# Kernel tuning notes

Measured on AMD Instinct MI355X. Metric: run time of the kernel, lower is better.

## Reference

```python
import jax, jax.numpy as jnp
import numpy as np

B, S, D, V = 32, 1024, 768, 32000


def setup_inputs() -> dict:
    key = jax.random.key(0)
    ks = jax.random.split(key, 12)
    scale = 0.02
    return {
        "tokens": jax.random.randint(ks[0], (B, S), 0, V, dtype=jnp.int32),
        "mask": jax.random.randint(ks[1], (B, S), 0, 2, dtype=jnp.int32),
        "emb": jax.random.normal(ks[2], (V, D), dtype=jnp.float32) * scale,
        "wq": jax.random.normal(ks[3], (D, D), dtype=jnp.float32) * scale,
        "wk": jax.random.normal(ks[4], (D, D), dtype=jnp.float32) * scale,
        "wv": jax.random.normal(ks[5], (D, D), dtype=jnp.float32) * scale,
        "ln_g": jnp.ones((D,), dtype=jnp.float32),
        "ln_b": jnp.zeros((D,), dtype=jnp.float32),
        "w1": jax.random.normal(ks[6], (D, D), dtype=jnp.float32) * scale,
        "b1": jnp.zeros((D,), dtype=jnp.float32),
        "wh": jax.random.normal(ks[7], (D, 2), dtype=jnp.float32) * scale,
        "bh": jnp.zeros((2,), dtype=jnp.float32),
    }


def reference(tokens, mask, emb, wq, wk, wv, ln_g, ln_b, w1, b1, wh, bh):
    # embedding lookup: [B,S,D]
    x = emb[tokens]
    q = x @ wq
    k = x @ wk
    v = x @ wv
    # unscaled attention scores: [B,S,S]
    s = jnp.einsum("bsd,btd->bst", q, k)
    # additive padding mask (mask==1 -> -1e9), broadcast over query dim
    s = s + (-1e9) * mask.astype(s.dtype)[:, None, :]
    a = jax.nn.softmax(s, axis=-1)
    o = jnp.einsum("bst,btd->bsd", a, v)
    # classify on first token
    cls = o[:, 0, :]  # [B,D]
    mu = jnp.mean(cls, axis=-1, keepdims=True)
    var = jnp.var(cls, axis=-1, keepdims=True)
    h = (cls - mu) * jax.lax.rsqrt(var + 1e-5) * ln_g + ln_b
    h = jax.nn.gelu(h @ w1 + b1, approximate=False)
    logits = h @ wh + bh  # [B,2]
    return (logits, a)
```

## Files before the change

### kernel.cpp

```cpp
#include <hip/hip_runtime.h>
#include <hip/hip_bf16.h>

#define NB 32
#define SS 1024
#define DD 768

typedef __attribute__((ext_vector_type(8))) short bf16x8;
typedef __attribute__((ext_vector_type(4))) float f32x4;

__device__ inline ushort f2bf(float f) {
    union { float f; unsigned u; } x;
    x.f = f;
    unsigned r = (x.u + 0x7fffu + ((x.u >> 16) & 1u)) >> 16;
    return (ushort)r;
}

#define GLOBAL_PTR(x) ((const __attribute__((address_space(1))) void*)(x))
#define LDS_PTR(x)    ((__attribute__((address_space(3))) void*)(x))

__global__ void k_cvt(const float* __restrict__ wq, const float* __restrict__ wk,
                      ushort* __restrict__ wqb, ushort* __restrict__ wkb) {
    const int i = (blockIdx.x * 256 + threadIdx.x) * 4;
    const float* src = blockIdx.y ? wk : wq;
    ushort* dst = blockIdx.y ? wkb : wqb;
    const float4 v = *(const float4*)(src + i);
    ushort4 o;
    o.x = f2bf(v.x); o.y = f2bf(v.y); o.z = f2bf(v.z); o.w = f2bf(v.w);
    *(ushort4*)(dst + i) = o;
}

__global__ void k_gather(const int* __restrict__ tokens, const float* __restrict__ emb,
                         ushort* __restrict__ xb) {
    int i = (blockIdx.x * 256 + threadIdx.x) * 4;
    int row = i / DD;
    int col = i - row * DD;
    int tok = tokens[row];
    const float4 v = *(const float4*)(emb + (size_t)tok * DD + col);
    ushort4 o;
    o.x = f2bf(v.x); o.y = f2bf(v.y); o.z = f2bf(v.z); o.w = f2bf(v.w);
    *(ushort4*)(xb + (size_t)row * DD + col) = o;
}

__global__ __launch_bounds__(256, 2) void k_gemm_s(const ushort* __restrict__ A,
                                                   const ushort* __restrict__ Bt,
                                                   ushort* __restrict__ Cb) {
    constexpr int BK = 64;
    __shared__ ushort As[2][128 * BK];
    __shared__ ushort Bs[2][128 * BK];
    const int tid = threadIdx.x;
    const int wave = tid >> 6, lane = tid & 63;
    const int bx = blockIdx.x, by = blockIdx.y;
    const size_t abase = (size_t)bx * 128 * DD;
    const size_t bbase = (size_t)by * 128 * DD;
    const int r = tid >> 3;
    const int cc = (tid & 7) * 8;

    auto stage = [&](int buf, int k0) {
#pragma unroll
        for (int i = 0; i < 4; i++) {
            __builtin_amdgcn_global_load_lds(GLOBAL_PTR(A + abase + (size_t)(r + i * 32) * DD + k0 + cc),
                                             LDS_PTR(&As[buf][(r + i * 32) * BK + cc]), 16, 0, 0);
            __builtin_amdgcn_global_load_lds(GLOBAL_PTR(Bt + bbase + (size_t)(r + i * 32) * DD + k0 + cc),
                                             LDS_PTR(&Bs[buf][(r + i * 32) * BK + cc]), 16, 0, 0);
        }
    };

    f32x4 acc[4][4] = {};
    const int wm = (wave >> 1) * 64, wn = (wave & 1) * 64;
    const int lr = lane & 15, lc = (lane >> 4) * 8;

    stage(0, 0);
    __syncthreads();
    int cur = 0;
#pragma unroll 1
    for (int k0 = 0; k0 < DD; k0 += BK) {
        if (k0 + BK < DD) stage(cur ^ 1, k0 + BK);
        const ushort* as = As[cur];
        const ushort* bs = Bs[cur];
#pragma unroll
        for (int kk = 0; kk < 2; kk++) {
            bf16x8 af[4], bfv[4];
#pragma unroll
            for (int m = 0; m < 4; m++)
                af[m] = *(const bf16x8*)(as + (wm + m * 16 + lr) * BK + kk * 32 + lc);
#pragma unroll
            for (int n = 0; n < 4; n++)
                bfv[n] = *(const bf16x8*)(bs + (wn + n * 16 + lr) * BK + kk * 32 + lc);
#pragma unroll
            for (int m = 0; m < 4; m++)
#pragma unroll
                for (int n = 0; n < 4; n++)
                    acc[m][n] = __builtin_amdgcn_mfma_f32_16x16x32_bf16(af[m], bfv[n], acc[m][n], 0, 0, 0);
        }
        __syncthreads();
        cur ^= 1;
    }
    const int rowbase = bx * 128 + wm + (lane >> 4) * 4;
    const int colbase = by * 128 + wn + (lane & 15);
#pragma unroll
    for (int m = 0; m < 4; m++)
#pragma unroll
        for (int n = 0; n < 4; n++)
#pragma unroll
            for (int j = 0; j < 4; j++)
                Cb[(size_t)(rowbase + m * 16 + j) * DD + colbase + n * 16] = f2bf(acc[m][n][j]);
}

__global__ __launch_bounds__(512) void k_attn(const ushort* __restrict__ Y,
                                              const ushort* __restrict__ X,
                                              const int* __restrict__ mask,
                                              float* __restrict__ Aout) {
    __shared__ ushort Bsh[2][SS * 32];
    __shared__ ushort Ash[2][64 * 32];
    __shared__ int    Msk[SS];
    __shared__ float  RedM[8][64];
    __shared__ float  RedS[8][64];

    const int tid = threadIdx.x;
    const int wid = tid >> 6, lane = tid & 63;
    const int la = lane & 15, lg = lane >> 4;

    const int wgid = blockIdx.x;
    const int g = wgid >> 7, w = wgid & 127;
    const int b = g * 8 + (w & 7);
    const int bx = w >> 3;
    const ushort* Ag = Y + (size_t)b * SS * DD + (size_t)bx * 64 * DD;
    const ushort* Bg = X + (size_t)b * SS * DD;
    float* Ao = Aout + (size_t)b * SS * SS + (size_t)bx * 64 * SS;

    Msk[tid] = mask[b * SS + tid];
    Msk[tid + 512] = mask[b * SS + tid + 512];

    auto stageB = [&](ushort* dst, const ushort* gsrc) {
#pragma unroll
        for (int l = 0; l < 8; l++) {
            const int L = (l * 512 + tid) * 16;
            const int r = L >> 6;
            const int scol = ((L & 63) ^ ((r & 3) << 4)) >> 1;
            __builtin_amdgcn_global_load_lds(GLOBAL_PTR(gsrc + (size_t)r * DD + scol),
                                             LDS_PTR(dst + (L >> 1)), 16, 0, 0);
        }
    };
    auto stageA = [&](ushort* dst, const ushort* gsrc) {
        if (tid < 256) {
            const int L = tid * 16;
            const int r = L >> 6;
            const int scol = ((L & 63) ^ ((r & 3) << 4)) >> 1;
            __builtin_amdgcn_global_load_lds(GLOBAL_PTR(gsrc + (size_t)r * DD + scol),
                                             LDS_PTR(dst + (L >> 1)), 16, 0, 0);
        }
    };

    const int koff = ((lg ^ (la & 3)) << 3);

    f32x4 acc[4][8] = {};

    stageA(&Ash[0][0], Ag);
    stageB(&Bsh[0][0], Bg);
    __syncthreads();

#pragma unroll 1
    for (int t = 0; t < 24; t++) {
        if (t < 23) {
            const int k1 = (t + 1) * 32;
            stageA(&Ash[(t + 1) & 1][0], Ag + k1);
            stageB(&Bsh[(t + 1) & 1][0], Bg + k1);
        }
        const ushort* ash = &Ash[t & 1][0];
        const ushort* bsh = &Bsh[t & 1][0];
        bf16x8 af[4];
#pragma unroll
        for (int m = 0; m < 4; m++)
            af[m] = *(const bf16x8*)(ash + (m * 16 + la) * 32 + koff);
#pragma unroll
        for (int n = 0; n < 8; n++) {
            const bf16x8 bf = *(const bf16x8*)(bsh + (wid * 128 + n * 16 + la) * 32 + koff);
            __builtin_amdgcn_s_setprio(1);
#pragma unroll
            for (int m = 0; m < 4; m++)
                acc[m][n] = __builtin_amdgcn_mfma_f32_16x16x32_bf16(af[m], bf, acc[m][n], 0, 0, 0);
            __builtin_amdgcn_s_setprio(0);
        }
        __syncthreads();
    }

    float bias[8];
#pragma unroll
    for (int n = 0; n < 8; n++)
        bias[n] = Msk[wid * 128 + n * 16 + la] ? -1e9f : 0.0f;

    float mxl[4][4];
#pragma unroll
    for (int m = 0; m < 4; m++)
#pragma unroll
        for (int j = 0; j < 4; j++) {
            float v = -3.4e38f;
#pragma unroll
            for (int n = 0; n < 8; n++) v = fmaxf(v, acc[m][n][j] + bias[n]);
#pragma unroll
            for (int off = 1; off < 16; off <<= 1) v = fmaxf(v, __shfl_xor(v, off));
            mxl[m][j] = v;
        }
    if (la == 0) {
#pragma unroll
        for (int m = 0; m < 4; m++)
#pragma unroll
            for (int j = 0; j < 4; j++)
                RedM[wid][m * 16 + lg * 4 + j] = mxl[m][j];
    }
    __syncthreads();
#pragma unroll
    for (int m = 0; m < 4; m++)
#pragma unroll
        for (int j = 0; j < 4; j++) {
            const int r = m * 16 + lg * 4 + j;
            float v = RedM[0][r];
#pragma unroll
            for (int ww = 1; ww < 8; ww++) v = fmaxf(v, RedM[ww][r]);
            mxl[m][j] = v;
        }

    float sml[4][4];
#pragma unroll
    for (int m = 0; m < 4; m++)
#pragma unroll
        for (int j = 0; j < 4; j++) {
            float s = 0.f;
#pragma unroll
            for (int n = 0; n < 8; n++) {
                const float e = __expf(acc[m][n][j] + bias[n] - mxl[m][j]);
                acc[m][n][j] = e;
                s += e;
            }
#pragma unroll
            for (int off = 1; off < 16; off <<= 1) s += __shfl_xor(s, off);
            sml[m][j] = s;
        }
    if (la == 0) {
#pragma unroll
        for (int m = 0; m < 4; m++)
#pragma unroll
            for (int j = 0; j < 4; j++)
                RedS[wid][m * 16 + lg * 4 + j] = sml[m][j];
    }
    __syncthreads();
#pragma unroll
    for (int m = 0; m < 4; m++)
#pragma unroll
        for (int j = 0; j < 4; j++) {
            const int r = m * 16 + lg * 4 + j;
            float s = RedS[0][r];
#pragma unroll
            for (int ww = 1; ww < 8; ww++) s += RedS[ww][r];
            const float inv = 1.0f / s;
#pragma unroll
            for (int n = 0; n < 8; n++)
                Ao[(size_t)r * SS + wid * 128 + n * 16 + la] = acc[m][n][j] * inv;
        }
}

__global__ __launch_bounds__(256) void k_xbar(const float* __restrict__ a, const int* __restrict__ tokens,
                                              const float* __restrict__ emb, float* __restrict__ part) {
    const int b = blockIdx.x >> 3, c = blockIdx.x & 7;
    __shared__ float a0s[128];
    __shared__ int toks[128];
    const int tid = threadIdx.x;
    if (tid < 128) {
        a0s[tid] = a[(size_t)b * SS * SS + c * 128 + tid];
        toks[tid] = tokens[b * SS + c * 128 + tid];
    }
    __syncthreads();
    float acc0 = 0.f, acc1 = 0.f, acc2 = 0.f;
#pragma unroll 4
    for (int t = 0; t < 128; t++) {
        const float at = a0s[t];
        const float* er = emb + (size_t)toks[t] * DD;
        acc0 = fmaf(at, er[tid], acc0);
        acc1 = fmaf(at, er[tid + 256], acc1);
        acc2 = fmaf(at, er[tid + 512], acc2);
    }
    float* p = part + ((size_t)c * NB + b) * DD;
    p[tid] = acc0; p[tid + 256] = acc1; p[tid + 512] = acc2;
}

__global__ __launch_bounds__(128) void k_cls(const float* __restrict__ part, const float* __restrict__ wv,
                                             float* __restrict__ cls) {
    const int b = blockIdx.y, tid = threadIdx.x;
    const int c = blockIdx.x * 128 + tid;
    __shared__ float xb[DD];
#pragma unroll
    for (int j = 0; j < 6; j++) {
        const int k = tid + j * 128;
        float s = 0.f;
#pragma unroll
        for (int p = 0; p < 8; p++) s += part[((size_t)p * NB + b) * DD + k];
        xb[k] = s;
    }
    __syncthreads();
    float acc = 0.f;
#pragma unroll 8
    for (int k = 0; k < DD; k++) acc = fmaf(xb[k], wv[(size_t)k * DD + c], acc);
    cls[(size_t)b * DD + c] = acc;
}

__device__ inline float block_sum256(float v, float* red, int tid) {
#pragma unroll
    for (int off = 32; off; off >>= 1) v += __shfl_xor(v, off);
    __syncthreads();
    if ((tid & 63) == 0) red[tid >> 6] = v;
    __syncthreads();
    return red[0] + red[1] + red[2] + red[3];
}

__global__ __launch_bounds__(256) void k_ln(const float* __restrict__ cls, const float* __restrict__ ln_g,
                                            const float* __restrict__ ln_b, float* __restrict__ hs) {
    const int b = blockIdx.x, tid = threadIdx.x;
    __shared__ float red[4];
    float v[3];
#pragma unroll
    for (int j = 0; j < 3; j++) v[j] = cls[(size_t)b * DD + tid + j * 256];
    const float mu = block_sum256(v[0] + v[1] + v[2], red, tid) * (1.0f / DD);
    float dv = 0.f;
#pragma unroll
    for (int j = 0; j < 3; j++) { const float d = v[j] - mu; dv += d * d; }
    __syncthreads();
    const float var = block_sum256(dv, red, tid) * (1.0f / DD);
    const float sc = 1.0f / sqrtf(var + 1e-5f);
#pragma unroll
    for (int j = 0; j < 3; j++) {
        const int d = tid + j * 256;
        hs[(size_t)b * DD + d] = (v[j] - mu) * sc * ln_g[d] + ln_b[d];
    }
}

__global__ __launch_bounds__(128) void k_mlp(const float* __restrict__ hs, const float* __restrict__ w1,
                                             const float* __restrict__ b1, const float* __restrict__ wh,
                                             float* __restrict__ part_l) {
    const int b = blockIdx.y, tid = threadIdx.x;
    const int j = blockIdx.x * 128 + tid;
    __shared__ float h[DD];
#pragma unroll
    for (int q = 0; q < 6; q++) h[tid + q * 128] = hs[(size_t)b * DD + tid + q * 128];
    __syncthreads();
    float p = b1[j];
#pragma unroll 8
    for (int d = 0; d < DD; d++) p = fmaf(h[d], w1[(size_t)d * DD + j], p);
    const float g = 0.5f * p * (1.0f + erff(p * 0.70710678118654752f));
    float l0 = g * wh[j * 2 + 0];
    float l1 = g * wh[j * 2 + 1];
#pragma unroll
    for (int off = 32; off; off >>= 1) { l0 += __shfl_xor(l0, off); l1 += __shfl_xor(l1, off); }
    __shared__ float r0[2], r1[2];
    if ((tid & 63) == 0) { r0[tid >> 6] = l0; r1[tid >> 6] = l1; }
    __syncthreads();
    if (tid == 0) {
        part_l[((size_t)b * 6 + blockIdx.x) * 2 + 0] = r0[0] + r0[1];
        part_l[((size_t)b * 6 + blockIdx.x) * 2 + 1] = r1[0] + r1[1];
    }
}

__global__ __launch_bounds__(64) void k_final(const float* __restrict__ part_l, const float* __restrict__ bh,
                                              float* __restrict__ out) {
    const int b = threadIdx.x;
    if (b < NB) {
        float l0 = bh[0], l1 = bh[1];
#pragma unroll
        for (int c = 0; c < 6; c++) {
            l0 += part_l[((size_t)b * 6 + c) * 2 + 0];
            l1 += part_l[((size_t)b * 6 + c) * 2 + 1];
        }
        out[b * 2 + 0] = l0;
        out[b * 2 + 1] = l1;
    }
}

extern "C" void kernel_launch(void* const* d_in, const int* in_sizes, int n_in,
                              void* d_out, int out_size, void* d_ws, size_t ws_size,
                              hipStream_t stream) {
    const int*   tokens = (const int*)d_in[0];
    const int*   mask   = (const int*)d_in[1];
    const float* emb    = (const float*)d_in[2];
    const float* wq     = (const float*)d_in[3];
    const float* wk     = (const float*)d_in[4];
    const float* wv     = (const float*)d_in[5];
    const float* ln_g   = (const float*)d_in[6];
    const float* ln_b   = (const float*)d_in[7];
    const float* w1     = (const float*)d_in[8];
    const float* b1     = (const float*)d_in[9];
    const float* wh     = (const float*)d_in[10];
    const float* bh     = (const float*)d_in[11];
    float* out = (float*)d_out;

    char* ws = (char*)d_ws;
    const size_t XB = (size_t)NB * SS * DD * 2;
    const size_t WB = (size_t)DD * DD * 2;
    ushort* xb  = (ushort*)ws;
    ushort* yb  = (ushort*)(ws + XB);
    ushort* wqb = (ushort*)(ws + 2 * XB);
    ushort* wkb = (ushort*)(ws + 2 * XB + WB);
    ushort* Wt  = (ushort*)(ws + 2 * XB + 2 * WB);
    char*   p4  = ws + 2 * XB + 3 * WB;
    float*  part   = (float*)p4;
    float*  cls    = (float*)(p4 + 786432);
    float*  hsb    = (float*)(p4 + 786432 + 98304);
    float*  part_l = (float*)(p4 + 786432 + 2 * 98304);

    float* a_region = out + 64;

    k_cvt<<<dim3(576, 2), 256, 0, stream>>>(wq, wk, wqb, wkb);
    k_gather<<<24576, 256, 0, stream>>>(tokens, emb, xb);
    k_gemm_s<<<dim3(6, 6), 256, 0, stream>>>(wkb, wqb, Wt);
    k_gemm_s<<<dim3(256, 6), 256, 0, stream>>>(xb, Wt, yb);
    k_attn<<<512, 512, 0, stream>>>(yb, xb, mask, a_region);
    k_xbar<<<256, 256, 0, stream>>>(a_region, tokens, emb, part);
    k_cls<<<dim3(6, NB), 128, 0, stream>>>(part, wv, cls);
    k_ln<<<NB, 256, 0, stream>>>(cls, ln_g, ln_b, hsb);
    k_mlp<<<dim3(6, NB), 128, 0, stream>>>(hsb, w1, b1, wh, part_l);
    k_final<<<1, 64, 0, stream>>>(part_l, bh, out);
}
```

Baseline: 348.8 us.

## Give each wave private LDS buffers and load A fragments directly from global

The QK^T main loop in the attention kernel now has each wave stage only its own 128-row slice of K into a per-wave double-buffered LDS region. Each wave loads its Q fragments straight from global into registers instead of staging them through shared LDS. This replaces the per-iteration workgroup __syncthreads with per-wave vmcnt waits, so waves no longer stall on each other. The trade-off is redundant global reads of the Q tile across the eight waves and more register pressure from two sets of A fragments.

```diff
diff --git a/kernel.cpp b/kernel.cpp
--- a/kernel.cpp
+++ b/kernel.cpp
@@ -110,8 +110,7 @@
                                               const ushort* __restrict__ X,
                                               const int* __restrict__ mask,
                                               float* __restrict__ Aout) {
-    __shared__ ushort Bsh[2][SS * 32];
-    __shared__ ushort Ash[2][64 * 32];
+    __shared__ ushort Bsh[8][2][128 * 32];
     __shared__ int    Msk[SS];
     __shared__ float  RedM[8][64];
     __shared__ float  RedS[8][64];
@@ -125,64 +124,64 @@
     const int b = g * 8 + (w & 7);
     const int bx = w >> 3;
     const ushort* Ag = Y + (size_t)b * SS * DD + (size_t)bx * 64 * DD;
-    const ushort* Bg = X + (size_t)b * SS * DD;
+    const ushort* Bg = X + (size_t)b * SS * DD + (size_t)wid * 128 * DD;
     float* Ao = Aout + (size_t)b * SS * SS + (size_t)bx * 64 * SS;
 
     Msk[tid] = mask[b * SS + tid];
     Msk[tid + 512] = mask[b * SS + tid + 512];
 
-    auto stageB = [&](ushort* dst, const ushort* gsrc) {
-#pragma unroll
-        for (int l = 0; l < 8; l++) {
-            const int L = (l * 512 + tid) * 16;
-            const int r = L >> 6;
-            const int scol = ((L & 63) ^ ((r & 3) << 4)) >> 1;
-            __builtin_amdgcn_global_load_lds(GLOBAL_PTR(gsrc + (size_t)r * DD + scol),
-                                             LDS_PTR(dst + (L >> 1)), 16, 0, 0);
-        }
+    const int sr = lane >> 2;
+    const int scc = ((lane & 3) ^ (sr & 3)) << 3;
+    const int koff = (lg ^ (la & 3)) << 3;
+
+    ushort* wb0 = &Bsh[wid][0][0];
+    ushort* wb1 = &Bsh[wid][1][0];
+
+    auto stageB = [&](ushort* dst, int k0) {
+#pragma unroll
+        for (int i = 0; i < 8; i++)
+            __builtin_amdgcn_global_load_lds(GLOBAL_PTR(Bg + (size_t)(i * 16 + sr) * DD + k0 + scc),
+                                             LDS_PTR(dst + i * 512), 16, 0, 0);
     };
-    auto stageA = [&](ushort* dst, const ushort* gsrc) {
-        if (tid < 256) {
-            const int L = tid * 16;
-            const int r = L >> 6;
-            const int scol = ((L & 63) ^ ((r & 3) << 4)) >> 1;
-            __builtin_amdgcn_global_load_lds(GLOBAL_PTR(gsrc + (size_t)r * DD + scol),
-                                             LDS_PTR(dst + (L >> 1)), 16, 0, 0);
-        }
+    auto loadA = [&](bf16x8* af, int k0) {
+#pragma unroll
+        for (int m = 0; m < 4; m++)
+            af[m] = *(const bf16x8*)(Ag + (size_t)(m * 16 + la) * DD + k0 + lg * 8);
     };
 
-    const int koff = ((lg ^ (la & 3)) << 3);
-
     f32x4 acc[4][8] = {};
-
-    stageA(&Ash[0][0], Ag);
-    stageB(&Bsh[0][0], Bg);
-    __syncthreads();
-
-#pragma unroll 1
-    for (int t = 0; t < 24; t++) {
-        if (t < 23) {
-            const int k1 = (t + 1) * 32;
-            stageA(&Ash[(t + 1) & 1][0], Ag + k1);
-            stageB(&Bsh[(t + 1) & 1][0], Bg + k1);
-        }
-        const ushort* ash = &Ash[t & 1][0];
-        const ushort* bsh = &Bsh[t & 1][0];
-        bf16x8 af[4];
-#pragma unroll
-        for (int m = 0; m < 4; m++)
-            af[m] = *(const bf16x8*)(ash + (m * 16 + la) * 32 + koff);
+    bf16x8 afA[4], afB[4];
+
+    auto comp = [&](const ushort* bsh, const bf16x8* af) {
 #pragma unroll
         for (int n = 0; n < 8; n++) {
-            const bf16x8 bf = *(const bf16x8*)(bsh + (wid * 128 + n * 16 + la) * 32 + koff);
+            const bf16x8 bf = *(const bf16x8*)(bsh + (n * 16 + la) * 32 + koff);
             __builtin_amdgcn_s_setprio(1);
 #pragma unroll
             for (int m = 0; m < 4; m++)
                 acc[m][n] = __builtin_amdgcn_mfma_f32_16x16x32_bf16(af[m], bf, acc[m][n], 0, 0, 0);
             __builtin_amdgcn_s_setprio(0);
         }
-        __syncthreads();
-    }
+    };
+
+    stageB(wb0, 0);
+    loadA(afA, 0);
+    asm volatile("s_waitcnt vmcnt(0)" ::: "memory");
+    __builtin_amdgcn_sched_barrier(0);
+
+#pragma unroll 1
+    for (int tt = 0; tt < 12; tt++) {
+        const int t0 = tt * 2;
+        if (t0 + 1 < 24) { stageB(wb1, (t0 + 1) * 32); loadA(afB, (t0 + 1) * 32); }
+        comp(wb0, afA);
+        asm volatile("s_waitcnt vmcnt(0)" ::: "memory");
+        __builtin_amdgcn_sched_barrier(0);
+        if (t0 + 2 < 24) { stageB(wb0, (t0 + 2) * 32); loadA(afA, (t0 + 2) * 32); }
+        comp(wb1, afB);
+        asm volatile("s_waitcnt vmcnt(0)" ::: "memory");
+        __builtin_amdgcn_sched_barrier(0);
+    }
+    __syncthreads();
 
     float bias[8];
 #pragma unroll
```

New measurement: 344.0 us. Within noise of the previous version (-1.4%).

## Enlarge attention workgroup to 128 query rows with 16 waves sharing K tile

Applied to the files above, without the earlier changes.

The attention score kernel now runs 1024-thread workgroups that each cover 128 query rows instead of 64. Sixteen waves are arranged 2x8 over rows and key columns, so every staged 1024x32 K slice in LDS serves twice as many query rows. This halves the global reloads of the K operand and halves the grid to 256 blocks. The cost is one block per CU with fewer blocks than CUs, less latency hiding across blocks, and larger barriers.

```diff
diff --git a/kernel.cpp b/kernel.cpp
--- a/kernel.cpp
+++ b/kernel.cpp
@@ -106,75 +106,73 @@
                 Cb[(size_t)(rowbase + m * 16 + j) * DD + colbase + n * 16] = f2bf(acc[m][n][j]);
 }
 
-__global__ __launch_bounds__(512) void k_attn(const ushort* __restrict__ Y,
-                                              const ushort* __restrict__ X,
-                                              const int* __restrict__ mask,
-                                              float* __restrict__ Aout) {
+__global__ __launch_bounds__(1024) void k_attn(const ushort* __restrict__ Y,
+                                               const ushort* __restrict__ X,
+                                               const int* __restrict__ mask,
+                                               float* __restrict__ Aout) {
     __shared__ ushort Bsh[2][SS * 32];
-    __shared__ ushort Ash[2][64 * 32];
+    __shared__ ushort Ash[2][128 * 32];
     __shared__ int    Msk[SS];
-    __shared__ float  RedM[8][64];
-    __shared__ float  RedS[8][64];
+    __shared__ float  RedM[8][128];
+    __shared__ float  RedS[8][128];
 
     const int tid = threadIdx.x;
     const int wid = tid >> 6, lane = tid & 63;
     const int la = lane & 15, lg = lane >> 4;
+    const int wm = wid & 1, wn = wid >> 1;
 
     const int wgid = blockIdx.x;
-    const int g = wgid >> 7, w = wgid & 127;
-    const int b = g * 8 + (w & 7);
-    const int bx = w >> 3;
-    const ushort* Ag = Y + (size_t)b * SS * DD + (size_t)bx * 64 * DD;
+    const int x = wgid & 7, k = wgid >> 3;
+    const int b = x + 8 * (k >> 3);
+    const int bx = k & 7;
+    const ushort* Ag = Y + (size_t)b * SS * DD + (size_t)bx * 128 * DD;
     const ushort* Bg = X + (size_t)b * SS * DD;
-    float* Ao = Aout + (size_t)b * SS * SS + (size_t)bx * 64 * SS;
+    float* Ao = Aout + (size_t)b * SS * SS + (size_t)bx * 128 * SS;
 
     Msk[tid] = mask[b * SS + tid];
-    Msk[tid + 512] = mask[b * SS + tid + 512];
-
-    auto stageB = [&](ushort* dst, const ushort* gsrc) {
-#pragma unroll
-        for (int l = 0; l < 8; l++) {
-            const int L = (l * 512 + tid) * 16;
-            const int r = L >> 6;
-            const int scol = ((L & 63) ^ ((r & 3) << 4)) >> 1;
-            __builtin_amdgcn_global_load_lds(GLOBAL_PTR(gsrc + (size_t)r * DD + scol),
-                                             LDS_PTR(dst + (L >> 1)), 16, 0, 0);
+
+    auto stageB = [&](ushort* dst, int k0) {
+#pragma unroll
+        for (int i = 0; i < 4; i++) {
+            const int idx = i * 1024 + tid;
+            const int r = idx >> 2;
+            const int scol = ((idx & 3) ^ (r & 3)) << 3;
+            __builtin_amdgcn_global_load_lds(GLOBAL_PTR(Bg + (size_t)r * DD + k0 + scol),
+                                             LDS_PTR(dst + idx * 8), 16, 0, 0);
         }
     };
-    auto stageA = [&](ushort* dst, const ushort* gsrc) {
-        if (tid < 256) {
-            const int L = tid * 16;
-            const int r = L >> 6;
-            const int scol = ((L & 63) ^ ((r & 3) << 4)) >> 1;
-            __builtin_amdgcn_global_load_lds(GLOBAL_PTR(gsrc + (size_t)r * DD + scol),
-                                             LDS_PTR(dst + (L >> 1)), 16, 0, 0);
+    auto stageA = [&](ushort* dst, int k0) {
+        if (tid < 512) {
+            const int r = tid >> 2;
+            const int scol = ((tid & 3) ^ (r & 3)) << 3;
+            __builtin_amdgcn_global_load_lds(GLOBAL_PTR(Ag + (size_t)r * DD + k0 + scol),
+                                             LDS_PTR(dst + tid * 8), 16, 0, 0);
         }
     };
 
-    const int koff = ((lg ^ (la & 3)) << 3);
+    const int koff = (lg ^ (la & 3)) << 3;
 
     f32x4 acc[4][8] = {};
 
-    stageA(&Ash[0][0], Ag);
-    stageB(&Bsh[0][0], Bg);
+    stageB(&Bsh[0][0], 0);
+    stageA(&Ash[0][0], 0);
     __syncthreads();
 
 #pragma unroll 1
     for (int t = 0; t < 24; t++) {
         if (t < 23) {
-            const int k1 = (t + 1) * 32;
-            stageA(&Ash[(t + 1) & 1][0], Ag + k1);
-            stageB(&Bsh[(t + 1) & 1][0], Bg + k1);
+            stageB(&Bsh[(t + 1) & 1][0], (t + 1) * 32);
+            stageA(&Ash[(t + 1) & 1][0], (t + 1) * 32);
         }
         const ushort* ash = &Ash[t & 1][0];
         const ushort* bsh = &Bsh[t & 1][0];
         bf16x8 af[4];
 #pragma unroll
         for (int m = 0; m < 4; m++)
-            af[m] = *(const bf16x8*)(ash + (m * 16 + la) * 32 + koff);
+            af[m] = *(const bf16x8*)(ash + (wm * 64 + m * 16 + la) * 32 + koff);
 #pragma unroll
         for (int n = 0; n < 8; n++) {
-            const bf16x8 bf = *(const bf16x8*)(bsh + (wid * 128 + n * 16 + la) * 32 + koff);
+            const bf16x8 bf = *(const bf16x8*)(bsh + (wn * 128 + n * 16 + la) * 32 + koff);
             __builtin_amdgcn_s_setprio(1);
 #pragma unroll
             for (int m = 0; m < 4; m++)
@@ -187,7 +185,7 @@
     float bias[8];
 #pragma unroll
     for (int n = 0; n < 8; n++)
-        bias[n] = Msk[wid * 128 + n * 16 + la] ? -1e9f : 0.0f;
+        bias[n] = Msk[wn * 128 + n * 16 + la] ? -1e9f : 0.0f;
 
     float mxl[4][4];
 #pragma unroll
@@ -206,14 +204,14 @@
         for (int m = 0; m < 4; m++)
 #pragma unroll
             for (int j = 0; j < 4; j++)
-                RedM[wid][m * 16 + lg * 4 + j] = mxl[m][j];
+                RedM[wn][wm * 64 + m * 16 + lg * 4 + j] = mxl[m][j];
     }
     __syncthreads();
 #pragma unroll
     for (int m = 0; m < 4; m++)
 #pragma unroll
         for (int j = 0; j < 4; j++) {
-            const int r = m * 16 + lg * 4 + j;
+            const int r = wm * 64 + m * 16 + lg * 4 + j;
             float v = RedM[0][r];
 #pragma unroll
             for (int ww = 1; ww < 8; ww++) v = fmaxf(v, RedM[ww][r]);
@@ -241,21 +239,21 @@
         for (int m = 0; m < 4; m++)
 #pragma unroll
             for (int j = 0; j < 4; j++)
-                RedS[wid][m * 16 + lg * 4 + j] = sml[m][j];
+                RedS[wn][wm * 64 + m * 16 + lg * 4 + j] = sml[m][j];
     }
     __syncthreads();
 #pragma unroll
     for (int m = 0; m < 4; m++)
 #pragma unroll
         for (int j = 0; j < 4; j++) {
-            const int r = m * 16 + lg * 4 + j;
+            const int r = wm * 64 + m * 16 + lg * 4 + j;
             float s = RedS[0][r];
 #pragma unroll
             for (int ww = 1; ww < 8; ww++) s += RedS[ww][r];
             const float inv = 1.0f / s;
 #pragma unroll
             for (int n = 0; n < 8; n++)
-                Ao[(size_t)r * SS + wid * 128 + n * 16 + la] = acc[m][n][j] * inv;
+                Ao[(size_t)r * SS + wn * 128 + n * 16 + la] = acc[m][n][j] * inv;
         }
 }
 
@@ -411,7 +409,7 @@
     k_gather<<<24576, 256, 0, stream>>>(tokens, emb, xb);
     k_gemm_s<<<dim3(6, 6), 256, 0, stream>>>(wkb, wqb, Wt);
     k_gemm_s<<<dim3(256, 6), 256, 0, stream>>>(xb, Wt, yb);
-    k_attn<<<512, 512, 0, stream>>>(yb, xb, mask, a_region);
+    k_attn<<<256, 1024, 0, stream>>>(yb, xb, mask, a_region);
     k_xbar<<<256, 256, 0, stream>>>(a_region, tokens, emb, part);
     k_cls<<<dim3(6, NB), 128, 0, stream>>>(part, wv, cls);
     k_ln<<<NB, 256, 0, stream>>>(cls, ln_g, ln_b, hsb);
```

Result: slower. 620.2 us (+77.8%).
